# Optimization experiments

Measured on AMD Instinct MI355X. Metric: run time of the kernel, lower is better.

Reference implementation:

```python
import jax, jax.numpy as jnp
import numpy as np

BATCH, SEQ = 1, 2048
D_MODEL, N_HEADS, D_HEAD = 2048, 16, 128
ROTARY_DIM = 128
N_CTX = 2048
EPS = 1e-5
IGNORE = -100000.0
ATTN_SCALE = float(np.sqrt(D_HEAD))  # use_attn_scale=True, no layer-idx scaling
ROTARY_BASE = 10000.0


def _ln_pre(x):
    # LayerNormPre: center and normalize, no learned scale/bias
    x = x - x.mean(axis=-1, keepdims=True)
    scale = jnp.sqrt((x * x).mean(axis=-1, keepdims=True) + EPS)
    return x / scale


def _sin_cos_rotary(rotary_dim, n_ctx, base=ROTARY_BASE):
    pos = jnp.arange(n_ctx, dtype=jnp.float32)
    dim = jnp.arange(rotary_dim // 2, dtype=jnp.float32)
    freq = base ** (dim / (rotary_dim / 2))
    freq = jnp.repeat(freq, 2)  # einops.repeat 'd -> (d 2)' (interleaved)
    angles = pos[:, None] / freq[None, :]  # [n_ctx, rotary_dim]
    return jnp.sin(angles), jnp.cos(angles)


def _rotate_every_two(x):
    x1 = x[..., 0::2]
    x2 = x[..., 1::2]
    return jnp.stack([-x2, x1], axis=-1).reshape(x.shape)


def _apply_rotary(x, sin, cos):
    # x: [batch, pos, head, d_head]
    n_pos = x.shape[1]
    x_rot = x[..., :ROTARY_DIM]
    x_pass = x[..., ROTARY_DIM:]
    c = cos[:n_pos][:, None, :]  # [pos, 1, rotary_dim] broadcasts over head
    s = sin[:n_pos][:, None, :]
    x_rotated = x_rot * c + _rotate_every_two(x_rot) * s
    return jnp.concatenate([x_rotated, x_pass], axis=-1)


def setup_inputs() -> dict:
    key = jax.random.key(0)
    ks = jax.random.split(key, 6)
    init_std = 0.02
    return {
        "resid_pre": jax.random.normal(ks[0], (BATCH, SEQ, D_MODEL), jnp.float32),
        "W_Q": jax.random.normal(ks[1], (N_HEADS, D_MODEL, D_HEAD), jnp.float32) * init_std,
        "W_K": jax.random.normal(ks[2], (N_HEADS, D_MODEL, D_HEAD), jnp.float32) * init_std,
        "W_V": jax.random.normal(ks[3], (N_HEADS, D_MODEL, D_HEAD), jnp.float32) * init_std,
        "W_O": jax.random.normal(ks[4], (N_HEADS, D_HEAD, D_MODEL), jnp.float32) * init_std,
        "b_Q": jnp.zeros((N_HEADS, D_HEAD), jnp.float32),
        "b_K": jnp.zeros((N_HEADS, D_HEAD), jnp.float32),
        "b_V": jnp.zeros((N_HEADS, D_HEAD), jnp.float32),
        "b_O": jnp.zeros((D_MODEL,), jnp.float32),
    }


def reference(resid_pre, W_Q, W_K, W_V, W_O, b_Q, b_K, b_V, b_O):
    sin, cos = _sin_cos_rotary(ROTARY_DIM, N_CTX)
    xn = _ln_pre(resid_pre)  # LayerNormPre applied to resid_pre for q, k, v
    q = jnp.einsum("bpd,hde->bphe", xn, W_Q) + b_Q
    k = jnp.einsum("bpd,hde->bphe", xn, W_K) + b_K
    v = jnp.einsum("bpd,hde->bphe", xn, W_V) + b_V
    q = _apply_rotary(q, sin, cos)
    k = _apply_rotary(k, sin, cos)
    # attn_scores: [batch, head, query_pos, key_pos]
    scores = jnp.einsum("bqhe,bkhe->bhqk", q, k) / ATTN_SCALE
    n_pos = resid_pre.shape[1]
    causal = jnp.tril(jnp.ones((n_pos, n_pos), dtype=bool))
    scores = jnp.where(causal, scores, jnp.float32(IGNORE))
    attn = jax.nn.softmax(scores, axis=-1)
    z = jnp.einsum("bkhe,bhqk->bqhe", v, attn)
    out = jnp.einsum("bqhe,hed->bqd", z, W_O) + b_O
    return out
```

## Files before the change

### kernel.cpp

```cpp
#include <hip/hip_runtime.h>
#include <hip/hip_bf16.h>

#define SEQ    2048
#define DM     2048
#define NH     16
#define DH     128
#define EPS    1e-5f
#define SCALE_INV 0.08838834764831845f
#define SC2LOG    0.12751744995f

typedef unsigned short u16;
typedef u16  u16x4  __attribute__((ext_vector_type(4)));
typedef u16  u16x8  __attribute__((ext_vector_type(8)));
typedef unsigned u32x4 __attribute__((ext_vector_type(4)));
typedef __bf16 bf16x8 __attribute__((ext_vector_type(8)));
typedef float f32x4 __attribute__((ext_vector_type(4)));

__device__ __forceinline__ u16 f2bf(float f) {
    unsigned int u = __builtin_bit_cast(unsigned int, f);
    u += 0x7fffu + ((u >> 16) & 1u);
    return (u16)(u >> 16);
}
__device__ __forceinline__ float bf2f(u16 v) {
    return __builtin_bit_cast(float, (unsigned)v << 16);
}
__device__ __forceinline__ bf16x8 as_bf(u16x8 v) { return __builtin_bit_cast(bf16x8, v); }

__device__ __forceinline__ void gload16(const u16* g, u16* l) {
    __builtin_amdgcn_global_load_lds(
        (const __attribute__((address_space(1))) unsigned int*)g,
        (__attribute__((address_space(3))) unsigned int*)l, 16, 0, 0);
}

#define VMCNT(N) asm volatile("s_waitcnt vmcnt(" #N ")" ::: "memory")
#define LGKMCNT0 asm volatile("s_waitcnt lgkmcnt(0)" ::: "memory")
#define SCHEDBAR __builtin_amdgcn_sched_barrier(0)
#define BARRIER  __builtin_amdgcn_s_barrier()

__global__ __launch_bounds__(256) void prep_kernel(const float* __restrict__ x,
                                                   const float* __restrict__ WQ,
                                                   const float* __restrict__ WK,
                                                   const float* __restrict__ WV,
                                                   const float* __restrict__ WO,
                                                   u16* __restrict__ xn,
                                                   float2* __restrict__ rope,
                                                   u16* __restrict__ outW,
                                                   u16* __restrict__ outWO) {
    __shared__ union {
        struct { float ss[4], qq[4]; } ln;
        u16 tile[64][65];
    } sm;
    int bid = blockIdx.x;
    int t = threadIdx.x;
    if (bid < SEQ) {
        int row = bid;
        if (t < 64) {
            float freq = powf(10000.f, (float)t * (1.f / 64.f));
            float ang = (float)row / freq;
            rope[row * 64 + t] = make_float2(sinf(ang), cosf(ang));
        }
        const float* xr = x + (size_t)row * DM;
        float4 v0 = *(const float4*)(xr + t * 4);
        float4 v1 = *(const float4*)(xr + 1024 + t * 4);
        float s = v0.x + v0.y + v0.z + v0.w + v1.x + v1.y + v1.z + v1.w;
        float q = v0.x*v0.x + v0.y*v0.y + v0.z*v0.z + v0.w*v0.w
                + v1.x*v1.x + v1.y*v1.y + v1.z*v1.z + v1.w*v1.w;
        #pragma unroll
        for (int o = 32; o; o >>= 1) { s += __shfl_xor(s, o); q += __shfl_xor(q, o); }
        if ((t & 63) == 0) { sm.ln.ss[t >> 6] = s; sm.ln.qq[t >> 6] = q; }
        __syncthreads();
        s = sm.ln.ss[0] + sm.ln.ss[1] + sm.ln.ss[2] + sm.ln.ss[3];
        q = sm.ln.qq[0] + sm.ln.qq[1] + sm.ln.qq[2] + sm.ln.qq[3];
        float mean = s * (1.f / DM);
        float var  = q * (1.f / DM) - mean * mean;
        float rstd = rsqrtf(var + EPS);
        u16* orow = xn + (size_t)row * DM;
        u16x4 o0 = { f2bf((v0.x-mean)*rstd), f2bf((v0.y-mean)*rstd),
                     f2bf((v0.z-mean)*rstd), f2bf((v0.w-mean)*rstd) };
        u16x4 o1 = { f2bf((v1.x-mean)*rstd), f2bf((v1.y-mean)*rstd),
                     f2bf((v1.z-mean)*rstd), f2bf((v1.w-mean)*rstd) };
        *(u16x4*)(orow + t * 4) = o0;
        *(u16x4*)(orow + 1024 + t * 4) = o1;
    } else {
        int tid = bid - SEQ;
        int bx = tid & 1, by = (tid >> 1) & 31, z = tid >> 6;
        const float* in;
        u16* o;
        int r0 = by * 64, c0;
        int inC, outC;
        if (z < 48) {
            int which = z >> 4, h = z & 15;
            in = ((which == 0) ? WQ : (which == 1) ? WK : WV) + (size_t)h * DM * DH;
            o  = outW + (size_t)z * DM * DH;
            c0 = bx * 64;
            inC = DH; outC = DM;
        } else {
            in = WO; o = outWO;
            c0 = ((z - 48) * 2 + bx) * 64;
            inC = DM; outC = DM;
        }
        #pragma unroll
        for (int it = 0; it < 4; ++it) {
            int idx = t + it * 256;
            int rr = idx >> 4, cc = (idx & 15) * 4;
            float4 v = *(const float4*)(in + (size_t)(r0 + rr) * inC + c0 + cc);
            sm.tile[rr][cc+0] = f2bf(v.x); sm.tile[rr][cc+1] = f2bf(v.y);
            sm.tile[rr][cc+2] = f2bf(v.z); sm.tile[rr][cc+3] = f2bf(v.w);
        }
        __syncthreads();
        #pragma unroll
        for (int it = 0; it < 4; ++it) {
            int idx = t + it * 256;
            int oc = idx >> 4, orr = (idx & 15) * 4;
            u16x4 w = { sm.tile[orr+0][oc], sm.tile[orr+1][oc],
                        sm.tile[orr+2][oc], sm.tile[orr+3][oc] };
            *(u16x4*)(o + (size_t)(c0 + oc) * outC + r0 + orr) = w;
        }
    }
}

__global__ __launch_bounds__(512, 2) void gemm_qkv(const u16* __restrict__ Xn,
                                                   const u16* __restrict__ Wt,
                                                   const float* __restrict__ bQ,
                                                   const float* __restrict__ bK,
                                                   const float* __restrict__ bV,
                                                   const float2* __restrict__ rope,
                                                   u16* __restrict__ qkv) {
    __shared__ u16 As[2][256 * 64], Bs[2][192 * 64];
    int id = blockIdx.x;
    int swz = (id & 7) * 32 + (id >> 3);
    int bx = swz & 7, by = swz >> 3;
    int m0 = bx * 256, n0 = by * 192;

    int t = threadIdx.x, lane = t & 63, wid = t >> 6;
    int wr = wid >> 2, wc = wid & 3;
    int cl = lane & 15, g = lane >> 4;

    auto stage = [&](int buf, int kt) {
        const u16* xa = Xn + (size_t)kt * 64;
        const u16* xb = Wt + (size_t)kt * 64;
        #pragma unroll
        for (int j = 0; j < 4; ++j) {
            int idx = t + j * 512;
            int row = idx >> 3;
            int slotS = (idx & 7) ^ (row & 7);
            gload16(xa + (size_t)(m0 + row) * DM + slotS * 8, &As[buf][idx * 8]);
        }
        #pragma unroll
        for (int j = 0; j < 3; ++j) {
            int idx = t + j * 512;
            int row = idx >> 3;
            int slotS = (idx & 7) ^ (row & 7);
            gload16(xb + (size_t)(n0 + row) * DM + slotS * 8, &Bs[buf][idx * 8]);
        }
    };

    f32x4 acc[8][3] = {};
    stage(0, 0);
    VMCNT(0);
    BARRIER;

    for (int kt = 0; kt < 32; ++kt) {
        int p = kt & 1;
        bool more = (kt + 1 < 32);
        bf16x8 bfr[3][2], af[4][2];
        #pragma unroll
        for (int nj = 0; nj < 3; ++nj)
            #pragma unroll
            for (int kk = 0; kk < 2; ++kk) {
                int row = wc * 48 + nj * 16 + cl;
                int s = (kk * 4 + g) ^ (row & 7);
                bfr[nj][kk] = as_bf(*(const u16x8*)&Bs[p][row * 64 + s * 8]);
            }
        #pragma unroll
        for (int mi = 0; mi < 4; ++mi)
            #pragma unroll
            for (int kk = 0; kk < 2; ++kk) {
                int row = wr * 128 + mi * 16 + cl;
                int s = (kk * 4 + g) ^ (row & 7);
                af[mi][kk] = as_bf(*(const u16x8*)&As[p][row * 64 + s * 8]);
            }
        if (more) stage(p ^ 1, kt + 1);
        __builtin_amdgcn_s_setprio(1);
        #pragma unroll
        for (int mi = 0; mi < 4; ++mi)
            #pragma unroll
            for (int nj = 0; nj < 3; ++nj)
                #pragma unroll
                for (int kk = 0; kk < 2; ++kk)
                    acc[mi][nj] = __builtin_amdgcn_mfma_f32_16x16x32_bf16(af[mi][kk], bfr[nj][kk], acc[mi][nj], 0, 0, 0);
        __builtin_amdgcn_s_setprio(0);
        #pragma unroll
        for (int mi = 0; mi < 4; ++mi)
            #pragma unroll
            for (int kk = 0; kk < 2; ++kk) {
                int row = wr * 128 + 64 + mi * 16 + cl;
                int s = (kk * 4 + g) ^ (row & 7);
                af[mi][kk] = as_bf(*(const u16x8*)&As[p][row * 64 + s * 8]);
            }
        __builtin_amdgcn_s_setprio(1);
        #pragma unroll
        for (int mi = 0; mi < 4; ++mi)
            #pragma unroll
            for (int nj = 0; nj < 3; ++nj)
                #pragma unroll
                for (int kk = 0; kk < 2; ++kk)
                    acc[4 + mi][nj] = __builtin_amdgcn_mfma_f32_16x16x32_bf16(af[mi][kk], bfr[nj][kk], acc[4 + mi][nj], 0, 0, 0);
        __builtin_amdgcn_s_setprio(0);
        VMCNT(0);
        SCHEDBAR;
        BARRIER;
    }

    #pragma unroll
    for (int i = 0; i < 8; ++i)
        #pragma unroll
        for (int nj = 0; nj < 3; ++nj) {
            int eg = n0 + wc * 48 + nj * 16 + cl;
            int which = eg >> 11;
            int h = (eg >> 7) & 15;
            int e = eg & 127;
            const float* bias = (which == 0) ? bQ : (which == 1) ? bK : bV;
            float bb = bias[h * DH + e];
            int p0 = m0 + wr * 128 + i * 16 + g * 4;
            if (which == 2) {
                u16* vbase = qkv + 2ll * NH * SEQ * DH + (size_t)h * DH * SEQ;
                u16x4 o = { f2bf(acc[i][nj][0] + bb), f2bf(acc[i][nj][1] + bb),
                            f2bf(acc[i][nj][2] + bb), f2bf(acc[i][nj][3] + bb) };
                *(u16x4*)(vbase + (size_t)e * SEQ + p0) = o;
            } else {
                u16* outbase = qkv + ((size_t)which * 16 + h) * SEQ * DH;
                #pragma unroll
                for (int r = 0; r < 4; ++r) {
                    int pp = p0 + r;
                    float v = acc[i][nj][r] + bb;
                    float pv = __shfl_xor(v, 1);
                    float2 sc2 = rope[pp * 64 + (e >> 1)];
                    v = (e & 1) ? (v * sc2.y + pv * sc2.x) : (v * sc2.y - pv * sc2.x);
                    outbase[(size_t)pp * DH + e] = f2bf(v);
                }
            }
        }
}

__device__ __forceinline__ int part_prefix(int j) {
    return (j < 16) ? 2 * (j - 8) : (j < 24 ? 16 + 3 * (j - 16) : 40 + 4 * (j - 24));
}

__global__ __launch_bounds__(256) void flash_kernel(const u16* __restrict__ Qg,
                                                    const u16* __restrict__ Kg,
                                                    const u16* __restrict__ Vt,
                                                    u16* __restrict__ Zg,
                                                    u16* __restrict__ pO,
                                                    float2* __restrict__ ml) {
    __shared__ u16 kt[64 * 128];
    __shared__ u16 vt[128 * 64];
    int h = blockIdx.x;
    int rem = blockIdx.y;
    int j = 31, c = 0;
    #pragma unroll 1
    for (int jj = 31; jj >= 0; --jj) {
        int ncj = (jj >> 3) + 1;
        if (rem < ncj) { j = jj; c = rem; break; }
        rem -= ncj;
    }
    int q0 = j * 64;
    int nc = (j >> 3) + 1;
    bool multi = (nc > 1);
    int kt0 = c * 8;
    int kt1 = min(j, c * 8 + 7);

    int t = threadIdx.x, lane = t & 63, w = t >> 6;
    int cl = lane & 15, g = lane >> 4;
    int qw0 = q0 + w * 16;
    const size_t hs = (size_t)h * SEQ;
    int src0 = cl + ((g & 1) << 5);
    int src1 = src0 + 16;
    bool hi = ((g >> 1) & 1) != 0;

    bf16x8 qf[4];
    #pragma unroll
    for (int st = 0; st < 4; ++st)
        qf[st] = as_bf(*(const u16x8*)(Qg + (hs + qw0 + cl) * DH + st * 32 + g * 8));

    f32x4 acc[8] = {};
    float mrun = -3e38f, lsum = 0.f;

    u16x8 kreg[4], vreg[4];
    auto load_tile = [&](int kv0) {
        #pragma unroll
        for (int jj = 0; jj < 4; ++jj) {
            int idx = t + jj * 256;
            kreg[jj] = *(const u16x8*)(Kg + (hs + kv0 + (idx >> 4)) * DH + (idx & 15) * 8);
            vreg[jj] = *(const u16x8*)(Vt + ((size_t)h * DH + (idx >> 3)) * SEQ + kv0 + (idx & 7) * 8);
        }
    };
    auto store_tile = [&]() {
        #pragma unroll
        for (int jj = 0; jj < 4; ++jj) {
            int idx = t + jj * 256;
            int row = idx >> 4, slot = idx & 15;
            *(u16x8*)((char*)kt + row * 256 + ((slot ^ (row & 7)) * 16)) = kreg[jj];
            int e = idx >> 3, ch = idx & 7;
            *(u16x8*)((char*)vt + e * 128 + ((ch ^ (e & 7)) * 16)) = vreg[jj];
        }
    };

    int kvbeg = kt0 * 64, kvend = kt1 * 64;
    load_tile(kvbeg);
    store_tile();

    for (int kv0 = kvbeg; kv0 <= kvend; kv0 += 64) {
        __syncthreads();
        bool more = (kv0 + 64 <= kvend);
        if (more) load_tile(kv0 + 64);

        f32x4 sc[4] = {};
        __builtin_amdgcn_s_setprio(1);
        #pragma unroll
        for (int st = 0; st < 4; ++st)
            #pragma unroll
            for (int cc = 0; cc < 4; ++cc) {
                int row = cc * 16 + cl;
                bf16x8 kf = as_bf(*(const u16x8*)((char*)kt + row * 256 + (((st * 4 + g) ^ (row & 7)) * 16)));
                sc[cc] = __builtin_amdgcn_mfma_f32_16x16x32_bf16(kf, qf[st], sc[cc], 0, 0, 0);
            }
        __builtin_amdgcn_s_setprio(0);

        bool needmask = (kv0 + 63 > qw0);
        int qrow = qw0 + cl;
        float pf[4][4];
        float tm = -3e38f;
        #pragma unroll
        for (int cc = 0; cc < 4; ++cc)
            #pragma unroll
            for (int r = 0; r < 4; ++r) {
                int kvq = kv0 + cc * 16 + g * 4 + r;
                float sval = sc[cc][r] * SC2LOG;
                if (needmask) sval = (kvq <= qrow) ? sval : -3e38f;
                pf[cc][r] = sval;
                tm = fmaxf(tm, sval);
            }
        tm = fmaxf(tm, __shfl_xor(tm, 16));
        tm = fmaxf(tm, __shfl_xor(tm, 32));

        if (!__all(tm <= mrun + 12.f)) {
            float mn = fmaxf(mrun, tm);
            float alpha = exp2f(mrun - mn);
            mrun = mn;
            lsum *= alpha;
            float aR[4];
            #pragma unroll
            for (int r = 0; r < 4; ++r) aR[r] = __shfl(alpha, g * 4 + r);
            #pragma unroll
            for (int n = 0; n < 8; ++n)
                #pragma unroll
                for (int r = 0; r < 4; ++r) acc[n][r] *= aR[r];
        }
        float rs = 0.f;
        #pragma unroll
        for (int cc = 0; cc < 4; ++cc)
            #pragma unroll
            for (int r = 0; r < 4; ++r) {
                float e2 = exp2f(pf[cc][r] - mrun);
                pf[cc][r] = e2;
                rs += e2;
            }
        rs += __shfl_xor(rs, 16);
        rs += __shfl_xor(rs, 32);
        lsum += rs;

        unsigned U[4][2];
        #pragma unroll
        for (int cc = 0; cc < 4; ++cc) {
            asm("v_cvt_pk_bf16_f32 %0, %1, %2" : "=v"(U[cc][0]) : "v"(pf[cc][0]), "v"(pf[cc][1]));
            asm("v_cvt_pk_bf16_f32 %0, %1, %2" : "=v"(U[cc][1]) : "v"(pf[cc][2]), "v"(pf[cc][3]));
        }
        unsigned wv[2][4];
        #pragma unroll
        for (int ks = 0; ks < 2; ++ks)
            #pragma unroll
            for (int hh = 0; hh < 2; ++hh) {
                unsigned e0 = (unsigned)__shfl((int)U[2*ks][hh],   src0);
                unsigned e1 = (unsigned)__shfl((int)U[2*ks][hh],   src1);
                unsigned o0 = (unsigned)__shfl((int)U[2*ks+1][hh], src0);
                unsigned o1 = (unsigned)__shfl((int)U[2*ks+1][hh], src1);
                wv[ks][hh]     = hi ? o0 : e0;
                wv[ks][2 + hh] = hi ? o1 : e1;
            }
        bf16x8 pa[2];
        {
            u32x4 w0 = { wv[0][0], wv[0][1], wv[0][2], wv[0][3] };
            u32x4 w1 = { wv[1][0], wv[1][1], wv[1][2], wv[1][3] };
            pa[0] = __builtin_bit_cast(bf16x8, w0);
            pa[1] = __builtin_bit_cast(bf16x8, w1);
        }

        __builtin_amdgcn_s_setprio(1);
        #pragma unroll
        for (int n = 0; n < 8; ++n)
            #pragma unroll
            for (int ks = 0; ks < 2; ++ks) {
                int e = n * 16 + cl;
                bf16x8 vf = as_bf(*(const u16x8*)((char*)vt + e * 128 + (((ks * 4 + g) ^ (e & 7)) * 16)));
                acc[n] = __builtin_amdgcn_mfma_f32_16x16x32_bf16(pa[ks], vf, acc[n], 0, 0, 0);
            }
        __builtin_amdgcn_s_setprio(0);

        if (!more) break;
        __syncthreads();
        store_tile();
    }

    if (multi) {
        int pidx = h * 72 + part_prefix(j) + c;
        if (lane < 16) ml[(size_t)pidx * 64 + w * 16 + cl] = make_float2(mrun, lsum);
        u16* po = pO + (size_t)pidx * (64 * 128);
        #pragma unroll
        for (int n = 0; n < 8; ++n)
            #pragma unroll
            for (int r = 0; r < 4; ++r)
                po[(w * 16 + g * 4 + r) * 128 + n * 16 + cl] = f2bf(acc[n][r]);
    } else {
        float inv = 1.0f / lsum;
        float invR[4];
        #pragma unroll
        for (int r = 0; r < 4; ++r) invR[r] = __shfl(inv, g * 4 + r);
        #pragma unroll
        for (int n = 0; n < 8; ++n)
            #pragma unroll
            for (int r = 0; r < 4; ++r) {
                int q = qw0 + g * 4 + r;
                Zg[(hs + q) * DH + n * 16 + cl] = f2bf(acc[n][r] * invR[r]);
            }
    }
}

__global__ __launch_bounds__(256) void merge_kernel(const u16* __restrict__ pO,
                                                    const float2* __restrict__ ml,
                                                    u16* __restrict__ Zg) {
    int h = blockIdx.x;
    int j = blockIdx.y + 8;
    int nc = (j >> 3) + 1;
    int pbase = h * 72 + part_prefix(j);
    int t = threadIdx.x;
    int row = t >> 2;
    int c0 = (t & 3) * 32;

    float mv[4], lv[4];
    float M = -3e38f;
    #pragma unroll
    for (int i = 0; i < 4; ++i) {
        int ii = (i < nc) ? i : 0;
        float2 mli = ml[(size_t)(pbase + ii) * 64 + row];
        mv[i] = mli.x; lv[i] = mli.y;
        if (i < nc) M = fmaxf(M, mli.x);
    }
    float wgt[4];
    float L = 0.f;
    #pragma unroll
    for (int i = 0; i < 4; ++i) {
        wgt[i] = (i < nc) ? exp2f(mv[i] - M) : 0.f;
        L += wgt[i] * lv[i];
    }
    float invL = 1.f / L;

    #pragma unroll
    for (int ccc = 0; ccc < 32; ccc += 8) {
        float o[8] = {};
        #pragma unroll
        for (int i = 0; i < 4; ++i) {
            int ii = (i < nc) ? i : 0;
            u16x8 v = *(const u16x8*)(pO + ((size_t)(pbase + ii) * 64 + row) * 128 + c0 + ccc);
            #pragma unroll
            for (int k = 0; k < 8; ++k) o[k] += wgt[i] * bf2f(v[k]);
        }
        u16x8 zv;
        #pragma unroll
        for (int k = 0; k < 8; ++k) zv[k] = f2bf(o[k] * invL);
        *(u16x8*)(Zg + ((size_t)h * SEQ + j * 64 + row) * DH + c0 + ccc) = zv;
    }
}

__global__ __launch_bounds__(256, 2) void gemm_out(const u16* __restrict__ Z,
                                                   const u16* __restrict__ Wot,
                                                   const float* __restrict__ bO,
                                                   float* __restrict__ out) {
    __shared__ u16 As[2][128 * 64], Bs[2][128 * 64];
    int id = blockIdx.x;
    int swz = (id & 7) * 32 + (id >> 3);
    int m0 = (swz & 15) * 128, n0 = (swz >> 4) * 128;
    int t = threadIdx.x, lane = t & 63, w = t >> 6;
    int wr = w >> 1, wc = w & 1;
    int cl = lane & 15, g = lane >> 4;

    auto stage = [&](int buf, int kt) {
        int k0 = kt * 64;
        int hh = k0 >> 7, e0 = k0 & 127;
        #pragma unroll
        for (int j = 0; j < 4; ++j) {
            int idx = t + j * 256;
            int row = idx >> 3;
            int slotS = (idx & 7) ^ (row & 7);
            gload16(Z + ((size_t)hh * SEQ + m0 + row) * DH + e0 + slotS * 8, &As[buf][idx * 8]);
            gload16(Wot + (size_t)(n0 + row) * DM + k0 + slotS * 8, &Bs[buf][idx * 8]);
        }
    };

    f32x4 acc[4][4] = {};
    stage(0, 0);
    VMCNT(0);
    BARRIER;
    for (int kt = 0; kt < 32; ++kt) {
        int p = kt & 1;
        bool more = (kt + 1 < 32);
        bf16x8 af[4][2], bfr[4][2];
        #pragma unroll
        for (int i = 0; i < 4; ++i)
            #pragma unroll
            for (int kk = 0; kk < 2; ++kk) {
                int rowA = wr * 64 + i * 16 + cl;
                af[i][kk] = as_bf(*(const u16x8*)&As[p][rowA * 64 + (((kk * 4 + g) ^ (rowA & 7)) * 8)]);
                int rowB = wc * 64 + i * 16 + cl;
                bfr[i][kk] = as_bf(*(const u16x8*)&Bs[p][rowB * 64 + (((kk * 4 + g) ^ (rowB & 7)) * 8)]);
            }
        if (more) stage(p ^ 1, kt + 1);
        __builtin_amdgcn_s_setprio(1);
        #pragma unroll
        for (int i = 0; i < 4; ++i)
            #pragma unroll
            for (int j = 0; j < 4; ++j)
                #pragma unroll
                for (int kk = 0; kk < 2; ++kk)
                    acc[i][j] = __builtin_amdgcn_mfma_f32_16x16x32_bf16(af[i][kk], bfr[j][kk], acc[i][j], 0, 0, 0);
        __builtin_amdgcn_s_setprio(0);
        VMCNT(0);
        SCHEDBAR;
        BARRIER;
    }
    #pragma unroll
    for (int i = 0; i < 4; ++i)
        #pragma unroll
        for (int j = 0; j < 4; ++j) {
            int col = n0 + wc * 64 + j * 16 + cl;
            float bb = bO[col];
            #pragma unroll
            for (int r = 0; r < 4; ++r) {
                int p = m0 + wr * 64 + i * 16 + g * 4 + r;
                out[(size_t)p * DM + col] = acc[i][j][r] + bb;
            }
        }
}

extern "C" void kernel_launch(void* const* d_in, const int* in_sizes, int n_in,
                              void* d_out, int out_size, void* d_ws, size_t ws_size,
                              hipStream_t stream) {
    const float* resid = (const float*)d_in[0];
    const float* WQ = (const float*)d_in[1];
    const float* WK = (const float*)d_in[2];
    const float* WV = (const float*)d_in[3];
    const float* WO = (const float*)d_in[4];
    const float* bQ = (const float*)d_in[5];
    const float* bK = (const float*)d_in[6];
    const float* bV = (const float*)d_in[7];
    const float* bO = (const float*)d_in[8];
    float* out = (float*)d_out;
    char* ws = (char*)d_ws;

    float2* rope = (float2*)(ws);
    u16* xn   = (u16*)(ws + (1ll  << 20));
    u16* Wt   = (u16*)(ws + (9ll  << 20));
    u16* Wot  = (u16*)(ws + (33ll << 20));
    u16* qkv  = (u16*)(ws + (41ll << 20));
    u16* z    = (u16*)(ws + (65ll << 20));
    u16* pO   = (u16*)(ws);
    float2* ml = (float2*)(ws + (20ll << 20));

    prep_kernel<<<SEQ + 4096, 256, 0, stream>>>(resid, WQ, WK, WV, WO, xn, rope, Wt, Wot);

    gemm_qkv<<<256, 512, 0, stream>>>(xn, Wt, bQ, bK, bV, rope, qkv);

    const u16* Qg = qkv;
    const u16* Kg = qkv + 1ll * NH * SEQ * DH;
    const u16* Vt = qkv + 2ll * NH * SEQ * DH;
    flash_kernel<<<dim3(NH, 80), 256, 0, stream>>>(Qg, Kg, Vt, z, pO, ml);
    merge_kernel<<<dim3(NH, 24), 256, 0, stream>>>(pO, ml, z);

    gemm_out<<<256, 256, 0, stream>>>(z, Wot, bO, out);
}
```

Baseline: 175.7 us.

## Retile QKV GEMM to 128x256 with triple-buffered LDS pipeline

Changes the QKV projection GEMM tile from 256x192 to 128x256 and launches 384 blocks instead of 256, so the grid covers more of the 256 CUs. It replaces the double-buffered loop (wait on all loads, then barrier at the end of each k-step) with a three-stage buffer that prefetches two k-steps ahead and waits only on the older loads. This is meant to hide global-load latency and improve CU coverage. In exchange, per-block register reuse drops (16 accumulators instead of 24), more total global traffic results from the smaller M tile, and launch bounds now allow only one block per CU.

```diff
diff --git a/kernel.cpp b/kernel.cpp
--- a/kernel.cpp
+++ b/kernel.cpp
@@ -119,18 +119,18 @@
     }
 }
 
-__global__ __launch_bounds__(512, 2) void gemm_qkv(const u16* __restrict__ Xn,
+__global__ __launch_bounds__(512, 1) void gemm_qkv(const u16* __restrict__ Xn,
                                                    const u16* __restrict__ Wt,
                                                    const float* __restrict__ bQ,
                                                    const float* __restrict__ bK,
                                                    const float* __restrict__ bV,
                                                    const float2* __restrict__ rope,
                                                    u16* __restrict__ qkv) {
-    __shared__ u16 As[2][256 * 64], Bs[2][192 * 64];
+    __shared__ u16 As[3][128 * 64], Bs[3][256 * 64];
     int id = blockIdx.x;
-    int swz = (id & 7) * 32 + (id >> 3);
-    int bx = swz & 7, by = swz >> 3;
-    int m0 = bx * 256, n0 = by * 192;
+    int swz = (id & 7) * 48 + (id >> 3);
+    int bx = swz & 15, by = swz >> 4;
+    int m0 = bx * 128, n0 = by * 256;
 
     int t = threadIdx.x, lane = t & 63, wid = t >> 6;
     int wr = wid >> 2, wc = wid & 3;
@@ -139,101 +139,90 @@
     auto stage = [&](int buf, int kt) {
         const u16* xa = Xn + (size_t)kt * 64;
         const u16* xb = Wt + (size_t)kt * 64;
+        #pragma unroll
+        for (int j = 0; j < 2; ++j) {
+            int idx = t + j * 512;
+            int row = idx >> 3;
+            int slotS = (idx & 7) ^ (row & 7);
+            gload16(xa + (size_t)(m0 + row) * DM + slotS * 8, &As[buf][idx * 8]);
+        }
         #pragma unroll
         for (int j = 0; j < 4; ++j) {
             int idx = t + j * 512;
             int row = idx >> 3;
             int slotS = (idx & 7) ^ (row & 7);
-            gload16(xa + (size_t)(m0 + row) * DM + slotS * 8, &As[buf][idx * 8]);
-        }
-        #pragma unroll
-        for (int j = 0; j < 3; ++j) {
-            int idx = t + j * 512;
-            int row = idx >> 3;
-            int slotS = (idx & 7) ^ (row & 7);
             gload16(xb + (size_t)(n0 + row) * DM + slotS * 8, &Bs[buf][idx * 8]);
         }
     };
 
-    f32x4 acc[8][3] = {};
+    f32x4 acc[4][4] = {};
     stage(0, 0);
-    VMCNT(0);
-    BARRIER;
+    stage(1, 1);
+    int buf = 0;
 
     for (int kt = 0; kt < 32; ++kt) {
-        int p = kt & 1;
-        bool more = (kt + 1 < 32);
-        bf16x8 bfr[3][2], af[4][2];
-        #pragma unroll
-        for (int nj = 0; nj < 3; ++nj)
+        if (kt < 31) { VMCNT(6); } else { VMCNT(0); }
+        SCHEDBAR;
+        BARRIER;
+        SCHEDBAR;
+
+        bf16x8 af[4][2], bfr[4][2];
+        #pragma unroll
+        for (int mi = 0; mi < 4; ++mi)
             #pragma unroll
             for (int kk = 0; kk < 2; ++kk) {
-                int row = wc * 48 + nj * 16 + cl;
+                int row = wr * 64 + mi * 16 + cl;
                 int s = (kk * 4 + g) ^ (row & 7);
-                bfr[nj][kk] = as_bf(*(const u16x8*)&Bs[p][row * 64 + s * 8]);
-            }
+                af[mi][kk] = as_bf(*(const u16x8*)&As[buf][row * 64 + s * 8]);
+            }
+        #pragma unroll
+        for (int nj = 0; nj < 4; ++nj)
+            #pragma unroll
+            for (int kk = 0; kk < 2; ++kk) {
+                int row = wc * 64 + nj * 16 + cl;
+                int s = (kk * 4 + g) ^ (row & 7);
+                bfr[nj][kk] = as_bf(*(const u16x8*)&Bs[buf][row * 64 + s * 8]);
+            }
+        if (kt + 2 < 32) {
+            int nbuf = buf + 2; if (nbuf >= 3) nbuf -= 3;
+            stage(nbuf, kt + 2);
+        }
+        __builtin_amdgcn_s_setprio(1);
         #pragma unroll
         for (int mi = 0; mi < 4; ++mi)
             #pragma unroll
-            for (int kk = 0; kk < 2; ++kk) {
-                int row = wr * 128 + mi * 16 + cl;
-                int s = (kk * 4 + g) ^ (row & 7);
-                af[mi][kk] = as_bf(*(const u16x8*)&As[p][row * 64 + s * 8]);
-            }
-        if (more) stage(p ^ 1, kt + 1);
-        __builtin_amdgcn_s_setprio(1);
-        #pragma unroll
-        for (int mi = 0; mi < 4; ++mi)
-            #pragma unroll
-            for (int nj = 0; nj < 3; ++nj)
+            for (int nj = 0; nj < 4; ++nj)
                 #pragma unroll
                 for (int kk = 0; kk < 2; ++kk)
                     acc[mi][nj] = __builtin_amdgcn_mfma_f32_16x16x32_bf16(af[mi][kk], bfr[nj][kk], acc[mi][nj], 0, 0, 0);
         __builtin_amdgcn_s_setprio(0);
-        #pragma unroll
-        for (int mi = 0; mi < 4; ++mi)
-            #pragma unroll
-            for (int kk = 0; kk < 2; ++kk) {
-                int row = wr * 128 + 64 + mi * 16 + cl;
-                int s = (kk * 4 + g) ^ (row & 7);
-                af[mi][kk] = as_bf(*(const u16x8*)&As[p][row * 64 + s * 8]);
-            }
-        __builtin_amdgcn_s_setprio(1);
-        #pragma unroll
-        for (int mi = 0; mi < 4; ++mi)
-            #pragma unroll
-            for (int nj = 0; nj < 3; ++nj)
-                #pragma unroll
-                for (int kk = 0; kk < 2; ++kk)
-                    acc[4 + mi][nj] = __builtin_amdgcn_mfma_f32_16x16x32_bf16(af[mi][kk], bfr[nj][kk], acc[4 + mi][nj], 0, 0, 0);
-        __builtin_amdgcn_s_setprio(0);
-        VMCNT(0);
+        LGKMCNT0;
         SCHEDBAR;
-        BARRIER;
+        buf = (buf + 1 == 3) ? 0 : buf + 1;
     }
 
     #pragma unroll
-    for (int i = 0; i < 8; ++i)
-        #pragma unroll
-        for (int nj = 0; nj < 3; ++nj) {
-            int eg = n0 + wc * 48 + nj * 16 + cl;
+    for (int mi = 0; mi < 4; ++mi)
+        #pragma unroll
+        for (int nj = 0; nj < 4; ++nj) {
+            int eg = n0 + wc * 64 + nj * 16 + cl;
             int which = eg >> 11;
             int h = (eg >> 7) & 15;
             int e = eg & 127;
             const float* bias = (which == 0) ? bQ : (which == 1) ? bK : bV;
             float bb = bias[h * DH + e];
-            int p0 = m0 + wr * 128 + i * 16 + g * 4;
+            int p0 = m0 + wr * 64 + mi * 16 + g * 4;
             if (which == 2) {
                 u16* vbase = qkv + 2ll * NH * SEQ * DH + (size_t)h * DH * SEQ;
-                u16x4 o = { f2bf(acc[i][nj][0] + bb), f2bf(acc[i][nj][1] + bb),
-                            f2bf(acc[i][nj][2] + bb), f2bf(acc[i][nj][3] + bb) };
+                u16x4 o = { f2bf(acc[mi][nj][0] + bb), f2bf(acc[mi][nj][1] + bb),
+                            f2bf(acc[mi][nj][2] + bb), f2bf(acc[mi][nj][3] + bb) };
                 *(u16x4*)(vbase + (size_t)e * SEQ + p0) = o;
             } else {
                 u16* outbase = qkv + ((size_t)which * 16 + h) * SEQ * DH;
                 #pragma unroll
                 for (int r = 0; r < 4; ++r) {
                     int pp = p0 + r;
-                    float v = acc[i][nj][r] + bb;
+                    float v = acc[mi][nj][r] + bb;
                     float pv = __shfl_xor(v, 1);
                     float2 sc2 = rope[pp * 64 + (e >> 1)];
                     v = (e & 1) ? (v * sc2.y + pv * sc2.x) : (v * sc2.y - pv * sc2.x);
@@ -578,7 +567,7 @@
 
     prep_kernel<<<SEQ + 4096, 256, 0, stream>>>(resid, WQ, WK, WV, WO, xn, rope, Wt, Wot);
 
-    gemm_qkv<<<256, 512, 0, stream>>>(xn, Wt, bQ, bK, bV, rope, qkv);
+    gemm_qkv<<<384, 512, 0, stream>>>(xn, Wt, bQ, bK, bV, rope, qkv);
 
     const u16* Qg = qkv;
     const u16* Kg = qkv + 1ll * NH * SEQ * DH;
```

Measured after the change: 191.2 us. +8.8%, slower.
